# Kernel tuning notes

Measured on AMD Instinct MI355X. Metric: run time of the kernel, lower is better.

## Reference

```python
import jax, jax.numpy as jnp
from jax import lax
import numpy as np

N_TOOLS = 50
DIM = 512
N_TOKENS = 8192
PARAM_DIM = 256


def setup_inputs() -> dict:
    key = jax.random.key(0)
    ks = jax.random.split(key, 8)
    s = 1.0 / np.sqrt(DIM)
    x = jax.random.normal(ks[0], (N_TOKENS, DIM), dtype=jnp.float32)
    router_w = jax.random.uniform(ks[1], (N_TOOLS, DIM), jnp.float32, -s, s)
    router_b = jax.random.uniform(ks[2], (N_TOOLS,), jnp.float32, -s, s)
    expert_w = jax.random.uniform(ks[3], (N_TOOLS, DIM, DIM), jnp.float32, -s, s)
    expert_b = jax.random.uniform(ks[4], (N_TOOLS, DIM), jnp.float32, -s, s)
    param_w = jax.random.uniform(ks[5], (PARAM_DIM, DIM), jnp.float32, -s, s)
    param_b = jax.random.uniform(ks[6], (PARAM_DIM,), jnp.float32, -s, s)
    return {"x": x, "router_w": router_w, "router_b": router_b,
            "expert_w": expert_w, "expert_b": expert_b,
            "param_w": param_w, "param_b": param_b}


def _moe_adapt(x, tool_idx, expert_w, expert_b):
    # Top-1 dispatch: for each expert i, y_i = x @ W_i.T + b_i, written only
    # where tool_idx == i. Scan over the fixed 50 experts (mirrors the torch
    # masked per-expert Linear loop) with masked select instead of scatter.
    def step(acc, wb):
        i, W, b = wb
        y = x @ W.T + b  # [N, dim]
        mask = (tool_idx == i)[:, None]
        return jnp.where(mask, y, acc), None

    init = jnp.zeros_like(x)
    acc, _ = lax.scan(step, init, (jnp.arange(N_TOOLS), expert_w, expert_b))
    return acc


def reference(x, router_w, router_b, expert_w, expert_b, param_w, param_b):
    tool_logits = x @ router_w.T + router_b            # [N, 50]
    tool_probs = jax.nn.softmax(tool_logits, axis=-1)   # [N, 50]
    tool_idx = jnp.argmax(tool_probs, axis=-1)          # [N] int
    adapted = _moe_adapt(x, tool_idx, expert_w, expert_b)  # [N, dim]
    params = x @ param_w.T + param_b                    # [N, 256]
    return (tool_idx, tool_probs, adapted, params)
```

## Files before the change

kernel.cpp:

```cpp
#include <hip/hip_runtime.h>
#include <hip/hip_bf16.h>
#include <math.h>

#define N_TOKENS 8192
#define DIM      512
#define N_TOOLS  50
#define PARAM_DIM 256
#define N_ROWBLK (N_TOKENS / 64)
#define MAX_BATCHES 128
#define TM 128
#define LDSS 72

typedef float  f32x4 __attribute__((ext_vector_type(4)));
typedef short  s16x8 __attribute__((ext_vector_type(8)));
typedef short  s16x4 __attribute__((ext_vector_type(4)));

#define WS_IDX     0
#define WS_COUNTS  8192
#define WS_CURSOR  8256
#define WS_OFFSETS 8320
#define WS_BE      8384
#define WS_BM0     8512
#define WS_NB      8640
#define WS_ORDER   8704
#define WS_PWH     16896
#define WS_RWH     82432
#define WS_RWL     98816
#define WS_XH      115200
#define WS_XL      2212352

__device__ inline float bf2f(short s) {
    return __uint_as_float(((unsigned)(unsigned short)s) << 16);
}

__device__ inline s16x4 pk4(float a, float b, float c, float d) {
    __hip_bfloat162 p0 = __float22bfloat162_rn(make_float2(a, b));
    __hip_bfloat162 p1 = __float22bfloat162_rn(make_float2(c, d));
    union { __hip_bfloat162 h; short2 s; } u0, u1;
    u0.h = p0; u1.h = p1;
    s16x4 r; r[0] = u0.s.x; r[1] = u0.s.y; r[2] = u1.s.x; r[3] = u1.s.y;
    return r;
}

#define CVT_XB  4096
#define CVT_PWB 128
#define CVT_RWB 32
#define CVT_GRID (CVT_XB + CVT_PWB + CVT_RWB + 1)
__global__ __launch_bounds__(256) void cvt_kernel(const float* __restrict__ x,
                                                  const float* __restrict__ pw,
                                                  const float* __restrict__ rw,
                                                  short* __restrict__ xh,
                                                  short* __restrict__ xl,
                                                  short* __restrict__ pwh,
                                                  short* __restrict__ rwh,
                                                  short* __restrict__ rwl,
                                                  int* __restrict__ counts) {
    int bid = blockIdx.x;
    int tid = threadIdx.x;
    if (bid < CVT_XB) {
        size_t i = ((size_t)bid * 256 + tid) * 4;
        float4 v = *(const float4*)&x[i];
        s16x4 h = pk4(v.x, v.y, v.z, v.w);
        s16x4 l = pk4(v.x - bf2f(h[0]), v.y - bf2f(h[1]),
                      v.z - bf2f(h[2]), v.w - bf2f(h[3]));
        *(s16x4*)&xh[i] = h;
        *(s16x4*)&xl[i] = l;
    } else if (bid < CVT_XB + CVT_PWB) {
        size_t i = ((size_t)(bid - CVT_XB) * 256 + tid) * 4;
        float4 v = *(const float4*)&pw[i];
        *(s16x4*)&pwh[i] = pk4(v.x, v.y, v.z, v.w);
    } else if (bid < CVT_XB + CVT_PWB + CVT_RWB) {
        int i = ((bid - CVT_XB - CVT_PWB) * 256 + tid) * 4;
        int row = i >> 9;
        float4 v = {0.f, 0.f, 0.f, 0.f};
        if (row < N_TOOLS) v = *(const float4*)&rw[i];
        s16x4 h = pk4(v.x, v.y, v.z, v.w);
        s16x4 l = pk4(v.x - bf2f(h[0]), v.y - bf2f(h[1]),
                      v.z - bf2f(h[2]), v.w - bf2f(h[3]));
        *(s16x4*)&rwh[i] = h;
        *(s16x4*)&rwl[i] = l;
    } else {
        if (tid < 64) counts[tid] = 0;
    }
}

__global__ __launch_bounds__(256) void head_mfma(const short* __restrict__ xh,
                                                 const short* __restrict__ xl,
                                                 const short* __restrict__ pwh,
                                                 const float* __restrict__ pb,
                                                 const short* __restrict__ rwh,
                                                 const short* __restrict__ rwl,
                                                 const float* __restrict__ rb,
                                                 float* __restrict__ out_params,
                                                 float* __restrict__ probs,
                                                 float* __restrict__ out_idx,
                                                 int* __restrict__ idx_i,
                                                 int* __restrict__ counts) {
    int r0 = blockIdx.y * 64;
    bool isl = (blockIdx.x == 4);
    int c0 = isl ? 0 : blockIdx.x * 64;

    __shared__ short As[64 * LDSS];
    __shared__ short Bs[64 * LDSS];
    __shared__ short Al[64 * LDSS];
    __shared__ short Bl[64 * LDSS];
    __shared__ int rowcol[64];

    int tid = threadIdx.x;
    int wv = tid >> 6;
    int lane = tid & 63;
    int fm = lane & 15;
    int q = lane >> 4;

    int ar0 = tid >> 3, ag = tid & 7;
    int ar1 = ar0 + 32;
    const short* aptr0 = xh + (size_t)(r0 + ar0) * DIM + ag * 8;
    const short* aptr1 = xh + (size_t)(r0 + ar1) * DIM + ag * 8;
    const short* alptr0 = xl + (size_t)(r0 + ar0) * DIM + ag * 8;
    const short* alptr1 = xl + (size_t)(r0 + ar1) * DIM + ag * 8;

    const short* bsrc = isl ? rwh : (pwh + (size_t)c0 * DIM);
    int bc[2], bg[2];
    const short* bph[2];
    const short* bpl[2];
#pragma unroll
    for (int i = 0; i < 2; ++i) {
        int u = i * 256 + tid;
        bc[i] = u >> 3; bg[i] = u & 7;
        bph[i] = bsrc + (size_t)bc[i] * DIM + bg[i] * 8;
        bpl[i] = rwl + (size_t)bc[i] * DIM + bg[i] * 8;
    }

    f32x4 acc[4] = {{0.f, 0.f, 0.f, 0.f}, {0.f, 0.f, 0.f, 0.f},
                    {0.f, 0.f, 0.f, 0.f}, {0.f, 0.f, 0.f, 0.f}};

    s16x8 apre0, apre1, alpre0, alpre1;
    s16x8 bpre[2], blpre[2];
    apre0 = *(const s16x8*)aptr0;
    apre1 = *(const s16x8*)aptr1;
    if (isl) { alpre0 = *(const s16x8*)alptr0; alpre1 = *(const s16x8*)alptr1; }
#pragma unroll
    for (int i = 0; i < 2; ++i) {
        bpre[i] = *(const s16x8*)bph[i];
        if (isl) blpre[i] = *(const s16x8*)bpl[i];
    }

    for (int k0 = 0; k0 < DIM; k0 += 64) {
        *(s16x8*)&As[ar0 * LDSS + ag * 8] = apre0;
        *(s16x8*)&As[ar1 * LDSS + ag * 8] = apre1;
#pragma unroll
        for (int i = 0; i < 2; ++i)
            *(s16x8*)&Bs[bc[i] * LDSS + bg[i] * 8] = bpre[i];
        if (isl) {
            *(s16x8*)&Al[ar0 * LDSS + ag * 8] = alpre0;
            *(s16x8*)&Al[ar1 * LDSS + ag * 8] = alpre1;
#pragma unroll
            for (int i = 0; i < 2; ++i)
                *(s16x8*)&Bl[bc[i] * LDSS + bg[i] * 8] = blpre[i];
        }
        __syncthreads();

        int kn = k0 + 64;
        if (kn < DIM) {
            apre0 = *(const s16x8*)(aptr0 + kn);
            apre1 = *(const s16x8*)(aptr1 + kn);
            if (isl) {
                alpre0 = *(const s16x8*)(alptr0 + kn);
                alpre1 = *(const s16x8*)(alptr1 + kn);
            }
#pragma unroll
            for (int i = 0; i < 2; ++i) {
                bpre[i] = *(const s16x8*)(bph[i] + kn);
                if (isl) blpre[i] = *(const s16x8*)(bpl[i] + kn);
            }
        }

#pragma unroll
        for (int kk = 0; kk < 64; kk += 32) {
            int ao = (wv * 16 + fm) * LDSS + kk + q * 8;
            s16x8 a = *(const s16x8*)&As[ao];
            if (!isl) {
#pragma unroll
                for (int n = 0; n < 4; ++n) {
                    s16x8 b = *(const s16x8*)&Bs[(n * 16 + fm) * LDSS + kk + q * 8];
                    acc[n] = __builtin_amdgcn_mfma_f32_16x16x32_bf16(a, b, acc[n], 0, 0, 0);
                }
            } else {
                s16x8 al = *(const s16x8*)&Al[ao];
#pragma unroll
                for (int n = 0; n < 4; ++n) {
                    int bo = (n * 16 + fm) * LDSS + kk + q * 8;
                    s16x8 b  = *(const s16x8*)&Bs[bo];
                    s16x8 bl = *(const s16x8*)&Bl[bo];
                    acc[n] = __builtin_amdgcn_mfma_f32_16x16x32_bf16(a,  b,  acc[n], 0, 0, 0);
                    acc[n] = __builtin_amdgcn_mfma_f32_16x16x32_bf16(a,  bl, acc[n], 0, 0, 0);
                    acc[n] = __builtin_amdgcn_mfma_f32_16x16x32_bf16(al, b,  acc[n], 0, 0, 0);
                }
            }
        }
        __syncthreads();
    }

    if (!isl) {
        float bias[4];
#pragma unroll
        for (int n = 0; n < 4; ++n) bias[n] = pb[c0 + n * 16 + fm];
#pragma unroll
        for (int r = 0; r < 4; ++r) {
            int row = r0 + wv * 16 + q * 4 + r;
            float* op = out_params + (size_t)row * PARAM_DIM + c0;
#pragma unroll
            for (int n = 0; n < 4; ++n) op[n * 16 + fm] = acc[n][r] + bias[n];
        }
    } else {
        float rbv[4];
#pragma unroll
        for (int n = 0; n < 4; ++n) {
            int c = n * 16 + fm;
            rbv[n] = (c < N_TOOLS) ? rb[c] : 0.f;
        }
#pragma unroll
        for (int rr = 0; rr < 4; ++rr) {
            int row_l = wv * 16 + q * 4 + rr;
            int row = r0 + row_l;
            float v[4];
            float vmax = -INFINITY; int vcol = N_TOOLS;
#pragma unroll
            for (int n = 0; n < 4; ++n) {
                int c = n * 16 + fm;
                v[n] = acc[n][rr] + rbv[n];
                if (c < N_TOOLS && v[n] > vmax) { vmax = v[n]; vcol = c; }
            }
#pragma unroll
            for (int s = 1; s < 16; s <<= 1) {
                float om = __shfl_xor(vmax, s, 64);
                int   oc = __shfl_xor(vcol, s, 64);
                if (om > vmax || (om == vmax && oc < vcol)) { vmax = om; vcol = oc; }
            }
            float e[4]; float esum = 0.f;
#pragma unroll
            for (int n = 0; n < 4; ++n) {
                int c = n * 16 + fm;
                e[n] = (c < N_TOOLS) ? expf(v[n] - vmax) : 0.f;
                esum += e[n];
            }
#pragma unroll
            for (int s = 1; s < 16; s <<= 1) esum += __shfl_xor(esum, s, 64);
            float inv = 1.f / esum;
#pragma unroll
            for (int n = 0; n < 4; ++n) {
                int c = n * 16 + fm;
                if (c < N_TOOLS) probs[(size_t)row * N_TOOLS + c] = e[n] * inv;
            }
            if (fm == 0) {
                out_idx[row] = (float)vcol;
                idx_i[row] = vcol;
                rowcol[row_l] = vcol;
            }
        }
        __syncthreads();
        if (wv == 0) {
            int myc = rowcol[lane];
            int cnt = 0;
            for (int e2 = 0; e2 < N_TOOLS; ++e2) {
                unsigned long long m = __ballot(myc == e2);
                if (lane == e2) cnt = __popcll(m);
            }
            if (lane < N_TOOLS && cnt > 0) atomicAdd(&counts[lane], cnt);
        }
    }
}

__global__ void plumb_kernel(const int* __restrict__ counts,
                             int* __restrict__ offsets,
                             int* __restrict__ cursor,
                             int* __restrict__ batch_e,
                             int* __restrict__ batch_m0,
                             int* __restrict__ nb_out) {
    int lane = threadIdx.x;
    int c = (lane < N_TOOLS) ? counts[lane] : 0;
    int pre = c;
#pragma unroll
    for (int s = 1; s < 64; s <<= 1) {
        int v = __shfl_up(pre, s, 64);
        if (lane >= s) pre += v;
    }
    if (lane < N_TOOLS) { offsets[lane] = pre - c; cursor[lane] = pre - c; }

    int nb_i = (lane < N_TOOLS) ? (c + TM - 1) / TM : 0;
    int pre2 = nb_i;
#pragma unroll
    for (int s = 1; s < 64; s <<= 1) {
        int v = __shfl_up(pre2, s, 64);
        if (lane >= s) pre2 += v;
    }
    int bstart = pre2 - nb_i;
    for (int b = 0; b < nb_i; ++b) {
        batch_e[bstart + b] = lane;
        batch_m0[bstart + b] = b * TM;
    }
    if (lane == 63) nb_out[0] = pre2;
}

__global__ __launch_bounds__(256) void reorder_kernel(const int* __restrict__ idx_i,
                                                      int* __restrict__ cursor,
                                                      int* __restrict__ order) {
    __shared__ int lcnt[N_TOOLS];
    __shared__ int lbase[N_TOOLS];
    int tid = threadIdx.x;
    if (tid < N_TOOLS) lcnt[tid] = 0;
    __syncthreads();
    int t = blockIdx.x * 256 + tid;
    int e = idx_i[t];
    int r = atomicAdd(&lcnt[e], 1);
    __syncthreads();
    if (tid < N_TOOLS && lcnt[tid] > 0) lbase[tid] = atomicAdd(&cursor[tid], lcnt[tid]);
    __syncthreads();
    order[lbase[e] + r] = t;
}

__global__ __launch_bounds__(256) void adapted_mfma(const short* __restrict__ xh,
                                                    const float* __restrict__ ew,
                                                    const float* __restrict__ eb,
                                                    const int* __restrict__ order,
                                                    const int* __restrict__ batch_e,
                                                    const int* __restrict__ batch_m0,
                                                    const int* __restrict__ nb_ptr,
                                                    const int* __restrict__ offsets,
                                                    const int* __restrict__ counts,
                                                    float* __restrict__ out) {
    int b = blockIdx.y;
    if (b >= nb_ptr[0]) return;
    int e = batch_e[b];
    int m0 = batch_m0[b];
    int c0 = blockIdx.x * 64;
    int start = offsets[e] + m0;
    int len = counts[e] - m0;
    if (len > TM) len = TM;

    __shared__ short As[TM * LDSS];
    __shared__ short Bs[64 * LDSS];
    __shared__ int toks[TM];

    int tid = threadIdx.x;
    if (tid < TM) toks[tid] = (tid < len) ? order[start + tid] : -1;
    __syncthreads();

    int wv = tid >> 6;
    int lane = tid & 63;
    int fm = lane & 15;
    int q = lane >> 4;

    const float* We = ew + (size_t)e * DIM * DIM;

    int ag = tid & 7;
    int ar[4]; const short* aptr[4];
#pragma unroll
    for (int i = 0; i < 4; ++i) {
        ar[i] = i * 32 + (tid >> 3);
        int tk = toks[ar[i]];
        aptr[i] = (tk >= 0) ? xh + (size_t)tk * DIM + ag * 8 : nullptr;
    }
    int bc[4], bg[4];
    const float* bptr[4];
#pragma unroll
    for (int i = 0; i < 4; ++i) {
        int u = i * 256 + tid;
        bc[i] = u >> 4; bg[i] = u & 15;
        bptr[i] = We + (size_t)(c0 + bc[i]) * DIM + bg[i] * 4;
    }

    f32x4 acc[8] = {{0.f,0.f,0.f,0.f},{0.f,0.f,0.f,0.f},{0.f,0.f,0.f,0.f},{0.f,0.f,0.f,0.f},
                    {0.f,0.f,0.f,0.f},{0.f,0.f,0.f,0.f},{0.f,0.f,0.f,0.f},{0.f,0.f,0.f,0.f}};

    const s16x8 z8 = {0, 0, 0, 0, 0, 0, 0, 0};
    s16x8 apre[4];
    float4 bpre[4];
#pragma unroll
    for (int i = 0; i < 4; ++i) apre[i] = aptr[i] ? *(const s16x8*)aptr[i] : z8;
#pragma unroll
    for (int i = 0; i < 4; ++i) bpre[i] = *(const float4*)bptr[i];

    for (int k0 = 0; k0 < DIM; k0 += 64) {
#pragma unroll
        for (int i = 0; i < 4; ++i)
            *(s16x8*)&As[ar[i] * LDSS + ag * 8] = apre[i];
#pragma unroll
        for (int i = 0; i < 4; ++i) {
            float4 v = bpre[i];
            *(s16x4*)&Bs[bc[i] * LDSS + bg[i] * 4] = pk4(v.x, v.y, v.z, v.w);
        }
        __syncthreads();

        int kn = k0 + 64;
        if (kn < DIM) {
#pragma unroll
            for (int i = 0; i < 4; ++i) apre[i] = aptr[i] ? *(const s16x8*)(aptr[i] + kn) : z8;
#pragma unroll
            for (int i = 0; i < 4; ++i) bpre[i] = *(const float4*)(bptr[i] + kn);
        }

#pragma unroll
        for (int kk = 0; kk < 64; kk += 32) {
            s16x8 a0 = *(const s16x8*)&As[(wv * 32 + fm) * LDSS + kk + q * 8];
            s16x8 a1 = *(const s16x8*)&As[(wv * 32 + 16 + fm) * LDSS + kk + q * 8];
#pragma unroll
            for (int n = 0; n < 4; ++n) {
                s16x8 bf = *(const s16x8*)&Bs[(n * 16 + fm) * LDSS + kk + q * 8];
                acc[n]     = __builtin_amdgcn_mfma_f32_16x16x32_bf16(a0, bf, acc[n],     0, 0, 0);
                acc[4 + n] = __builtin_amdgcn_mfma_f32_16x16x32_bf16(a1, bf, acc[4 + n], 0, 0, 0);
            }
        }
        __syncthreads();
    }

    float bias[4];
#pragma unroll
    for (int n = 0; n < 4; ++n) bias[n] = eb[(size_t)e * DIM + c0 + n * 16 + fm];

#pragma unroll
    for (int m = 0; m < 2; ++m) {
#pragma unroll
        for (int r = 0; r < 4; ++r) {
            int row = wv * 32 + m * 16 + q * 4 + r;
            int tok = toks[row];
            if (tok < 0) continue;
            float* op = out + (size_t)tok * DIM + c0;
#pragma unroll
            for (int n = 0; n < 4; ++n) op[n * 16 + fm] = acc[m * 4 + n][r] + bias[n];
        }
    }
}

extern "C" void kernel_launch(void* const* d_in, const int* in_sizes, int n_in,
                              void* d_out, int out_size, void* d_ws, size_t ws_size,
                              hipStream_t stream) {
    const float* x        = (const float*)d_in[0];
    const float* router_w = (const float*)d_in[1];
    const float* router_b = (const float*)d_in[2];
    const float* expert_w = (const float*)d_in[3];
    const float* expert_b = (const float*)d_in[4];
    const float* param_w  = (const float*)d_in[5];
    const float* param_b  = (const float*)d_in[6];

    float* out = (float*)d_out;
    float* out_idx     = out;
    float* out_probs   = out + N_TOKENS;
    float* out_adapted = out + N_TOKENS + N_TOKENS * N_TOOLS;
    float* out_params  = out_adapted + (size_t)N_TOKENS * DIM;

    int* ws = (int*)d_ws;
    int* ws_idx     = ws + WS_IDX;
    int* ws_counts  = ws + WS_COUNTS;
    int* ws_cursor  = ws + WS_CURSOR;
    int* ws_offsets = ws + WS_OFFSETS;
    int* ws_be      = ws + WS_BE;
    int* ws_bm0     = ws + WS_BM0;
    int* ws_nb      = ws + WS_NB;
    int* ws_order   = ws + WS_ORDER;
    short* ws_pwh   = (short*)(ws + WS_PWH);
    short* ws_rwh   = (short*)(ws + WS_RWH);
    short* ws_rwl   = (short*)(ws + WS_RWL);
    short* ws_xh    = (short*)(ws + WS_XH);
    short* ws_xl    = (short*)(ws + WS_XL);

    cvt_kernel<<<CVT_GRID, 256, 0, stream>>>(x, param_w, router_w,
                                             ws_xh, ws_xl, ws_pwh, ws_rwh, ws_rwl,
                                             ws_counts);

    head_mfma<<<dim3(5, N_ROWBLK), 256, 0, stream>>>(ws_xh, ws_xl, ws_pwh, param_b,
                                                     ws_rwh, ws_rwl, router_b,
                                                     out_params, out_probs,
                                                     out_idx, ws_idx, ws_counts);

    plumb_kernel<<<1, 64, 0, stream>>>(ws_counts, ws_offsets, ws_cursor,
                                       ws_be, ws_bm0, ws_nb);

    reorder_kernel<<<N_TOKENS / 256, 256, 0, stream>>>(ws_idx, ws_cursor, ws_order);

    adapted_mfma<<<dim3(8, MAX_BATCHES), 256, 0, stream>>>(ws_xh, expert_w, expert_b,
                                                           ws_order, ws_be, ws_bm0, ws_nb,
                                                           ws_offsets, ws_counts, out_adapted);
}
```

Measured before the change: 152.3 us.

## Fuse x conversion into head GEMM, single-block sort, larger expert tiles

The standalone x-to-bf16 hi/lo conversion pass is removed. The head kernel now reads fp32 x directly, converts it in registers, computes the lo part only for the router tile, and writes the bf16 x copy from one column tile. Counting, prefix and reorder collapse into one 1024-thread sort kernel that uses ballot ranks, replacing the atomics plus the plumb and reorder kernels. The expert GEMM tile grows to 256 rows with 16 accumulators per wave, and both grids are remapped for XCD locality. The sort now runs in a single block, and the bigger tiles add register pressure and padding work for small experts.

```diff
diff --git a/kernel.cpp b/kernel.cpp
--- a/kernel.cpp
+++ b/kernel.cpp
@@ -7,8 +7,8 @@
 #define N_TOOLS  50
 #define PARAM_DIM 256
 #define N_ROWBLK (N_TOKENS / 64)
-#define MAX_BATCHES 128
-#define TM 128
+#define MAX_BATCHES 96
+#define TM 256
 #define LDSS 72
 
 typedef float  f32x4 __attribute__((ext_vector_type(4)));
@@ -16,18 +16,16 @@
 typedef short  s16x4 __attribute__((ext_vector_type(4)));
 
 #define WS_IDX     0
-#define WS_COUNTS  8192
-#define WS_CURSOR  8256
-#define WS_OFFSETS 8320
-#define WS_BE      8384
-#define WS_BM0     8512
-#define WS_NB      8640
-#define WS_ORDER   8704
-#define WS_PWH     16896
-#define WS_RWH     82432
-#define WS_RWL     98816
-#define WS_XH      115200
-#define WS_XL      2212352
+#define WS_OFFSETS 8192
+#define WS_COUNTS  8256
+#define WS_BE      8320
+#define WS_BM0     8416
+#define WS_NB      8512
+#define WS_ORDER   8528
+#define WS_PWH     16720
+#define WS_RWH     82256
+#define WS_RWL     98640
+#define WS_XH      115024
 
 __device__ inline float bf2f(short s) {
     return __uint_as_float(((unsigned)(unsigned short)s) << 16);
@@ -42,35 +40,42 @@
     return r;
 }
 
-#define CVT_XB  4096
+__device__ inline s16x8 pk8(float4 a, float4 b) {
+    s16x4 lo = pk4(a.x, a.y, a.z, a.w);
+    s16x4 hi = pk4(b.x, b.y, b.z, b.w);
+    s16x8 r;
+    r[0] = lo[0]; r[1] = lo[1]; r[2] = lo[2]; r[3] = lo[3];
+    r[4] = hi[0]; r[5] = hi[1]; r[6] = hi[2]; r[7] = hi[3];
+    return r;
+}
+
+__device__ inline s16x8 pk8lo(float4 a, float4 b, s16x8 h) {
+    s16x4 lo = pk4(a.x - bf2f(h[0]), a.y - bf2f(h[1]),
+                   a.z - bf2f(h[2]), a.w - bf2f(h[3]));
+    s16x4 hi = pk4(b.x - bf2f(h[4]), b.y - bf2f(h[5]),
+                   b.z - bf2f(h[6]), b.w - bf2f(h[7]));
+    s16x8 r;
+    r[0] = lo[0]; r[1] = lo[1]; r[2] = lo[2]; r[3] = lo[3];
+    r[4] = hi[0]; r[5] = hi[1]; r[6] = hi[2]; r[7] = hi[3];
+    return r;
+}
+
 #define CVT_PWB 128
 #define CVT_RWB 32
-#define CVT_GRID (CVT_XB + CVT_PWB + CVT_RWB + 1)
-__global__ __launch_bounds__(256) void cvt_kernel(const float* __restrict__ x,
-                                                  const float* __restrict__ pw,
-                                                  const float* __restrict__ rw,
-                                                  short* __restrict__ xh,
-                                                  short* __restrict__ xl,
-                                                  short* __restrict__ pwh,
-                                                  short* __restrict__ rwh,
-                                                  short* __restrict__ rwl,
-                                                  int* __restrict__ counts) {
+#define CVT_GRID (CVT_PWB + CVT_RWB)
+__global__ __launch_bounds__(256) void cvtB_kernel(const float* __restrict__ pw,
+                                                   const float* __restrict__ rw,
+                                                   short* __restrict__ pwh,
+                                                   short* __restrict__ rwh,
+                                                   short* __restrict__ rwl) {
     int bid = blockIdx.x;
     int tid = threadIdx.x;
-    if (bid < CVT_XB) {
+    if (bid < CVT_PWB) {
         size_t i = ((size_t)bid * 256 + tid) * 4;
-        float4 v = *(const float4*)&x[i];
-        s16x4 h = pk4(v.x, v.y, v.z, v.w);
-        s16x4 l = pk4(v.x - bf2f(h[0]), v.y - bf2f(h[1]),
-                      v.z - bf2f(h[2]), v.w - bf2f(h[3]));
-        *(s16x4*)&xh[i] = h;
-        *(s16x4*)&xl[i] = l;
-    } else if (bid < CVT_XB + CVT_PWB) {
-        size_t i = ((size_t)(bid - CVT_XB) * 256 + tid) * 4;
         float4 v = *(const float4*)&pw[i];
         *(s16x4*)&pwh[i] = pk4(v.x, v.y, v.z, v.w);
-    } else if (bid < CVT_XB + CVT_PWB + CVT_RWB) {
-        int i = ((bid - CVT_XB - CVT_PWB) * 256 + tid) * 4;
+    } else {
+        int i = ((bid - CVT_PWB) * 256 + tid) * 4;
         int row = i >> 9;
         float4 v = {0.f, 0.f, 0.f, 0.f};
         if (row < N_TOOLS) v = *(const float4*)&rw[i];
@@ -79,13 +84,10 @@
                       v.z - bf2f(h[2]), v.w - bf2f(h[3]));
         *(s16x4*)&rwh[i] = h;
         *(s16x4*)&rwl[i] = l;
-    } else {
-        if (tid < 64) counts[tid] = 0;
-    }
-}
-
-__global__ __launch_bounds__(256) void head_mfma(const short* __restrict__ xh,
-                                                 const short* __restrict__ xl,
+    }
+}
+
+__global__ __launch_bounds__(256) void head_mfma(const float* __restrict__ x,
                                                  const short* __restrict__ pwh,
                                                  const float* __restrict__ pb,
                                                  const short* __restrict__ rwh,
@@ -95,16 +97,22 @@
                                                  float* __restrict__ probs,
                                                  float* __restrict__ out_idx,
                                                  int* __restrict__ idx_i,
-                                                 int* __restrict__ counts) {
-    int r0 = blockIdx.y * 64;
-    bool isl = (blockIdx.x == 4);
-    int c0 = isl ? 0 : blockIdx.x * 64;
+                                                 short* __restrict__ xh) {
+    int bid = blockIdx.x;
+    int xcd = bid & 7;
+    int g = bid >> 3;
+    int tl = g % 5;
+    int yy = (g / 5) * 8 + xcd;
+
+    int r0 = yy * 64;
+    bool isl = (tl == 4);
+    bool isw = (tl == 0);
+    int c0 = isl ? 0 : tl * 64;
 
     __shared__ short As[64 * LDSS];
     __shared__ short Bs[64 * LDSS];
     __shared__ short Al[64 * LDSS];
     __shared__ short Bl[64 * LDSS];
-    __shared__ int rowcol[64];
 
     int tid = threadIdx.x;
     int wv = tid >> 6;
@@ -114,10 +122,10 @@
 
     int ar0 = tid >> 3, ag = tid & 7;
     int ar1 = ar0 + 32;
-    const short* aptr0 = xh + (size_t)(r0 + ar0) * DIM + ag * 8;
-    const short* aptr1 = xh + (size_t)(r0 + ar1) * DIM + ag * 8;
-    const short* alptr0 = xl + (size_t)(r0 + ar0) * DIM + ag * 8;
-    const short* alptr1 = xl + (size_t)(r0 + ar1) * DIM + ag * 8;
+    const float* xp0 = x + (size_t)(r0 + ar0) * DIM + ag * 8;
+    const float* xp1 = x + (size_t)(r0 + ar1) * DIM + ag * 8;
+    short* xo0 = xh + (size_t)(r0 + ar0) * DIM + ag * 8;
+    short* xo1 = xh + (size_t)(r0 + ar1) * DIM + ag * 8;
 
     const short* bsrc = isl ? rwh : (pwh + (size_t)c0 * DIM);
     int bc[2], bg[2];
@@ -134,11 +142,10 @@
     f32x4 acc[4] = {{0.f, 0.f, 0.f, 0.f}, {0.f, 0.f, 0.f, 0.f},
                     {0.f, 0.f, 0.f, 0.f}, {0.f, 0.f, 0.f, 0.f}};
 
-    s16x8 apre0, apre1, alpre0, alpre1;
+    float4 xa0, xb0, xa1, xb1;
     s16x8 bpre[2], blpre[2];
-    apre0 = *(const s16x8*)aptr0;
-    apre1 = *(const s16x8*)aptr1;
-    if (isl) { alpre0 = *(const s16x8*)alptr0; alpre1 = *(const s16x8*)alptr1; }
+    xa0 = *(const float4*)xp0; xb0 = *(const float4*)(xp0 + 4);
+    xa1 = *(const float4*)xp1; xb1 = *(const float4*)(xp1 + 4);
 #pragma unroll
     for (int i = 0; i < 2; ++i) {
         bpre[i] = *(const s16x8*)bph[i];
@@ -146,14 +153,22 @@
     }
 
     for (int k0 = 0; k0 < DIM; k0 += 64) {
-        *(s16x8*)&As[ar0 * LDSS + ag * 8] = apre0;
-        *(s16x8*)&As[ar1 * LDSS + ag * 8] = apre1;
+        s16x8 h0 = pk8(xa0, xb0);
+        s16x8 h1 = pk8(xa1, xb1);
+        *(s16x8*)&As[ar0 * LDSS + ag * 8] = h0;
+        *(s16x8*)&As[ar1 * LDSS + ag * 8] = h1;
+        if (isl) {
+            *(s16x8*)&Al[ar0 * LDSS + ag * 8] = pk8lo(xa0, xb0, h0);
+            *(s16x8*)&Al[ar1 * LDSS + ag * 8] = pk8lo(xa1, xb1, h1);
+        }
+        if (isw) {
+            *(s16x8*)(xo0 + k0) = h0;
+            *(s16x8*)(xo1 + k0) = h1;
+        }
 #pragma unroll
         for (int i = 0; i < 2; ++i)
             *(s16x8*)&Bs[bc[i] * LDSS + bg[i] * 8] = bpre[i];
         if (isl) {
-            *(s16x8*)&Al[ar0 * LDSS + ag * 8] = alpre0;
-            *(s16x8*)&Al[ar1 * LDSS + ag * 8] = alpre1;
 #pragma unroll
             for (int i = 0; i < 2; ++i)
                 *(s16x8*)&Bl[bc[i] * LDSS + bg[i] * 8] = blpre[i];
@@ -162,12 +177,8 @@
 
         int kn = k0 + 64;
         if (kn < DIM) {
-            apre0 = *(const s16x8*)(aptr0 + kn);
-            apre1 = *(const s16x8*)(aptr1 + kn);
-            if (isl) {
-                alpre0 = *(const s16x8*)(alptr0 + kn);
-                alpre1 = *(const s16x8*)(alptr1 + kn);
-            }
+            xa0 = *(const float4*)(xp0 + kn); xb0 = *(const float4*)(xp0 + kn + 4);
+            xa1 = *(const float4*)(xp1 + kn); xb1 = *(const float4*)(xp1 + kn + 4);
 #pragma unroll
             for (int i = 0; i < 2; ++i) {
                 bpre[i] = *(const s16x8*)(bph[i] + kn);
@@ -221,8 +232,7 @@
         }
 #pragma unroll
         for (int rr = 0; rr < 4; ++rr) {
-            int row_l = wv * 16 + q * 4 + rr;
-            int row = r0 + row_l;
+            int row = r0 + wv * 16 + q * 4 + rr;
             float v[4];
             float vmax = -INFINITY; int vcol = N_TOOLS;
 #pragma unroll
@@ -255,68 +265,84 @@
             if (fm == 0) {
                 out_idx[row] = (float)vcol;
                 idx_i[row] = vcol;
-                rowcol[row_l] = vcol;
-            }
-        }
-        __syncthreads();
-        if (wv == 0) {
-            int myc = rowcol[lane];
-            int cnt = 0;
-            for (int e2 = 0; e2 < N_TOOLS; ++e2) {
-                unsigned long long m = __ballot(myc == e2);
-                if (lane == e2) cnt = __popcll(m);
-            }
-            if (lane < N_TOOLS && cnt > 0) atomicAdd(&counts[lane], cnt);
-        }
-    }
-}
-
-__global__ void plumb_kernel(const int* __restrict__ counts,
-                             int* __restrict__ offsets,
-                             int* __restrict__ cursor,
-                             int* __restrict__ batch_e,
-                             int* __restrict__ batch_m0,
-                             int* __restrict__ nb_out) {
-    int lane = threadIdx.x;
-    int c = (lane < N_TOOLS) ? counts[lane] : 0;
-    int pre = c;
-#pragma unroll
-    for (int s = 1; s < 64; s <<= 1) {
-        int v = __shfl_up(pre, s, 64);
-        if (lane >= s) pre += v;
-    }
-    if (lane < N_TOOLS) { offsets[lane] = pre - c; cursor[lane] = pre - c; }
-
-    int nb_i = (lane < N_TOOLS) ? (c + TM - 1) / TM : 0;
-    int pre2 = nb_i;
-#pragma unroll
-    for (int s = 1; s < 64; s <<= 1) {
-        int v = __shfl_up(pre2, s, 64);
-        if (lane >= s) pre2 += v;
-    }
-    int bstart = pre2 - nb_i;
-    for (int b = 0; b < nb_i; ++b) {
-        batch_e[bstart + b] = lane;
-        batch_m0[bstart + b] = b * TM;
-    }
-    if (lane == 63) nb_out[0] = pre2;
-}
-
-__global__ __launch_bounds__(256) void reorder_kernel(const int* __restrict__ idx_i,
-                                                      int* __restrict__ cursor,
-                                                      int* __restrict__ order) {
-    __shared__ int lcnt[N_TOOLS];
-    __shared__ int lbase[N_TOOLS];
+            }
+        }
+    }
+}
+
+__global__ __launch_bounds__(1024) void sort_kernel(const int* __restrict__ idx,
+                                                    int* __restrict__ offsets,
+                                                    int* __restrict__ counts,
+                                                    int* __restrict__ order,
+                                                    int* __restrict__ batch_e,
+                                                    int* __restrict__ batch_m0,
+                                                    int* __restrict__ nb_out) {
+    __shared__ int cnt[128][N_TOOLS];
+    __shared__ int offs[64];
     int tid = threadIdx.x;
-    if (tid < N_TOOLS) lcnt[tid] = 0;
+    int w = tid >> 6;
+    int lane = tid & 63;
+    unsigned long long lt = (1ull << lane) - 1ull;
+
+    int myE[8], myRank[8];
+#pragma unroll
+    for (int r = 0; r < 8; ++r) {
+        int t = w * 512 + r * 64 + lane;
+        int e = idx[t];
+        myE[r] = e;
+        int rank = 0, c = 0;
+        for (int ex = 0; ex < N_TOOLS; ++ex) {
+            unsigned long long m = __ballot(e == ex);
+            if (e == ex) rank = __popcll(m & lt);
+            if (lane == ex) c = __popcll(m);
+        }
+        myRank[r] = rank;
+        if (lane < N_TOOLS) cnt[w * 8 + r][lane] = c;
+    }
     __syncthreads();
-    int t = blockIdx.x * 256 + tid;
-    int e = idx_i[t];
-    int r = atomicAdd(&lcnt[e], 1);
+
+    if (tid < 64) {
+        int base = 0;
+        if (tid < N_TOOLS) {
+            for (int i = 0; i < 128; ++i) {
+                int tmp = cnt[i][tid];
+                cnt[i][tid] = base;
+                base += tmp;
+            }
+        }
+        int c = base;
+        int pre = c;
+#pragma unroll
+        for (int s = 1; s < 64; s <<= 1) {
+            int v = __shfl_up(pre, s, 64);
+            if (tid >= s) pre += v;
+        }
+        int off = pre - c;
+        offs[tid] = off;
+        if (tid < N_TOOLS) { offsets[tid] = off; counts[tid] = c; }
+
+        int nb_i = (tid < N_TOOLS) ? (c + TM - 1) / TM : 0;
+        int pre2 = nb_i;
+#pragma unroll
+        for (int s = 1; s < 64; s <<= 1) {
+            int v = __shfl_up(pre2, s, 64);
+            if (tid >= s) pre2 += v;
+        }
+        int bstart = pre2 - nb_i;
+        for (int b = 0; b < nb_i; ++b) {
+            batch_e[bstart + b] = tid;
+            batch_m0[bstart + b] = b * TM;
+        }
+        if (tid == 63) nb_out[0] = pre2;
+    }
     __syncthreads();
-    if (tid < N_TOOLS && lcnt[tid] > 0) lbase[tid] = atomicAdd(&cursor[tid], lcnt[tid]);
-    __syncthreads();
-    order[lbase[e] + r] = t;
+
+#pragma unroll
+    for (int r = 0; r < 8; ++r) {
+        int t = w * 512 + r * 64 + lane;
+        int e = myE[r];
+        order[offs[e] + cnt[w * 8 + r][e] + myRank[r]] = t;
+    }
 }
 
 __global__ __launch_bounds__(256) void adapted_mfma(const short* __restrict__ xh,
@@ -329,11 +355,15 @@
                                                     const int* __restrict__ offsets,
                                                     const int* __restrict__ counts,
                                                     float* __restrict__ out) {
-    int b = blockIdx.y;
+    int bid = blockIdx.x;
+    int x8 = bid & 7;
+    int u = bid >> 3;
+    int ct = u & 7;
+    int b = (bid >> 6) * 8 + x8;
     if (b >= nb_ptr[0]) return;
     int e = batch_e[b];
     int m0 = batch_m0[b];
-    int c0 = blockIdx.x * 64;
+    int c0 = ct * 64;
     int start = offsets[e] + m0;
     int len = counts[e] - m0;
     if (len > TM) len = TM;
@@ -343,7 +373,7 @@
     __shared__ int toks[TM];
 
     int tid = threadIdx.x;
-    if (tid < TM) toks[tid] = (tid < len) ? order[start + tid] : -1;
+    toks[tid] = (tid < len) ? order[start + tid] : -1;
     __syncthreads();
 
     int wv = tid >> 6;
@@ -354,37 +384,38 @@
     const float* We = ew + (size_t)e * DIM * DIM;
 
     int ag = tid & 7;
-    int ar[4]; const short* aptr[4];
-#pragma unroll
-    for (int i = 0; i < 4; ++i) {
-        ar[i] = i * 32 + (tid >> 3);
-        int tk = toks[ar[i]];
+    int arr = tid >> 3;
+    const short* aptr[8];
+#pragma unroll
+    for (int i = 0; i < 8; ++i) {
+        int tk = toks[i * 32 + arr];
         aptr[i] = (tk >= 0) ? xh + (size_t)tk * DIM + ag * 8 : nullptr;
     }
     int bc[4], bg[4];
     const float* bptr[4];
 #pragma unroll
     for (int i = 0; i < 4; ++i) {
-        int u = i * 256 + tid;
-        bc[i] = u >> 4; bg[i] = u & 15;
+        int u2 = i * 256 + tid;
+        bc[i] = u2 >> 4; bg[i] = u2 & 15;
         bptr[i] = We + (size_t)(c0 + bc[i]) * DIM + bg[i] * 4;
     }
 
-    f32x4 acc[8] = {{0.f,0.f,0.f,0.f},{0.f,0.f,0.f,0.f},{0.f,0.f,0.f,0.f},{0.f,0.f,0.f,0.f},
-                    {0.f,0.f,0.f,0.f},{0.f,0.f,0.f,0.f},{0.f,0.f,0.f,0.f},{0.f,0.f,0.f,0.f}};
+    f32x4 acc[16];
+#pragma unroll
+    for (int i = 0; i < 16; ++i) acc[i] = (f32x4){0.f, 0.f, 0.f, 0.f};
 
     const s16x8 z8 = {0, 0, 0, 0, 0, 0, 0, 0};
-    s16x8 apre[4];
+    s16x8 apre[8];
     float4 bpre[4];
 #pragma unroll
-    for (int i = 0; i < 4; ++i) apre[i] = aptr[i] ? *(const s16x8*)aptr[i] : z8;
+    for (int i = 0; i < 8; ++i) apre[i] = aptr[i] ? *(const s16x8*)aptr[i] : z8;
 #pragma unroll
     for (int i = 0; i < 4; ++i) bpre[i] = *(const float4*)bptr[i];
 
     for (int k0 = 0; k0 < DIM; k0 += 64) {
 #pragma unroll
-        for (int i = 0; i < 4; ++i)
-            *(s16x8*)&As[ar[i] * LDSS + ag * 8] = apre[i];
+        for (int i = 0; i < 8; ++i)
+            *(s16x8*)&As[(i * 32 + arr) * LDSS + ag * 8] = apre[i];
 #pragma unroll
         for (int i = 0; i < 4; ++i) {
             float4 v = bpre[i];
@@ -395,20 +426,23 @@
         int kn = k0 + 64;
         if (kn < DIM) {
 #pragma unroll
-            for (int i = 0; i < 4; ++i) apre[i] = aptr[i] ? *(const s16x8*)(aptr[i] + kn) : z8;
+            for (int i = 0; i < 8; ++i) apre[i] = aptr[i] ? *(const s16x8*)(aptr[i] + kn) : z8;
 #pragma unroll
             for (int i = 0; i < 4; ++i) bpre[i] = *(const float4*)(bptr[i] + kn);
         }
 
 #pragma unroll
         for (int kk = 0; kk < 64; kk += 32) {
-            s16x8 a0 = *(const s16x8*)&As[(wv * 32 + fm) * LDSS + kk + q * 8];
-            s16x8 a1 = *(const s16x8*)&As[(wv * 32 + 16 + fm) * LDSS + kk + q * 8];
+            s16x8 a[4];
+#pragma unroll
+            for (int m = 0; m < 4; ++m)
+                a[m] = *(const s16x8*)&As[(wv * 64 + m * 16 + fm) * LDSS + kk + q * 8];
 #pragma unroll
             for (int n = 0; n < 4; ++n) {
-                s16x8 bf = *(const s16x8*)&Bs[(n * 16 + fm) * LDSS + kk + q * 8];
-                acc[n]     = __builtin_amdgcn_mfma_f32_16x16x32_bf16(a0, bf, acc[n],     0, 0, 0);
-                acc[4 + n] = __builtin_amdgcn_mfma_f32_16x16x32_bf16(a1, bf, acc[4 + n], 0, 0, 0);
+                s16x8 bfv = *(const s16x8*)&Bs[(n * 16 + fm) * LDSS + kk + q * 8];
+#pragma unroll
+                for (int m = 0; m < 4; ++m)
+                    acc[n * 4 + m] = __builtin_amdgcn_mfma_f32_16x16x32_bf16(a[m], bfv, acc[n * 4 + m], 0, 0, 0);
             }
         }
         __syncthreads();
@@ -419,15 +453,15 @@
     for (int n = 0; n < 4; ++n) bias[n] = eb[(size_t)e * DIM + c0 + n * 16 + fm];
 
 #pragma unroll
-    for (int m = 0; m < 2; ++m) {
+    for (int m = 0; m < 4; ++m) {
 #pragma unroll
         for (int r = 0; r < 4; ++r) {
-            int row = wv * 32 + m * 16 + q * 4 + r;
+            int row = wv * 64 + m * 16 + q * 4 + r;
             int tok = toks[row];
             if (tok < 0) continue;
             float* op = out + (size_t)tok * DIM + c0;
 #pragma unroll
-            for (int n = 0; n < 4; ++n) op[n * 16 + fm] = acc[m * 4 + n][r] + bias[n];
+            for (int n = 0; n < 4; ++n) op[n * 16 + fm] = acc[n * 4 + m][r] + bias[n];
         }
     }
 }
@@ -451,9 +485,8 @@
 
     int* ws = (int*)d_ws;
     int* ws_idx     = ws + WS_IDX;
+    int* ws_offsets = ws + WS_OFFSETS;
     int* ws_counts  = ws + WS_COUNTS;
-    int* ws_cursor  = ws + WS_CURSOR;
-    int* ws_offsets = ws + WS_OFFSETS;
     int* ws_be      = ws + WS_BE;
     int* ws_bm0     = ws + WS_BM0;
     int* ws_nb      = ws + WS_NB;
@@ -462,23 +495,16 @@
     short* ws_rwh   = (short*)(ws + WS_RWH);
     short* ws_rwl   = (short*)(ws + WS_RWL);
     short* ws_xh    = (short*)(ws + WS_XH);
-    short* ws_xl    = (short*)(ws + WS_XL);
-
-    cvt_kernel<<<CVT_GRID, 256, 0, stream>>>(x, param_w, router_w,
-                                             ws_xh, ws_xl, ws_pwh, ws_rwh, ws_rwl,
-                                             ws_counts);
-
-    head_mfma<<<dim3(5, N_ROWBLK), 256, 0, stream>>>(ws_xh, ws_xl, ws_pwh, param_b,
-                                                     ws_rwh, ws_rwl, router_b,
-                                                     out_params, out_probs,
-                                                     out_idx, ws_idx, ws_counts);
-
-    plumb_kernel<<<1, 64, 0, stream>>>(ws_counts, ws_offsets, ws_cursor,
-                                       ws_be, ws_bm0, ws_nb);
-
-    reorder_kernel<<<N_TOKENS / 256, 256, 0, stream>>>(ws_idx, ws_cursor, ws_order);
-
-    adapted_mfma<<<dim3(8, MAX_BATCHES), 256, 0, stream>>>(ws_xh, expert_w, expert_b,
-                                                           ws_order, ws_be, ws_bm0, ws_nb,
-                                                           ws_offsets, ws_counts, out_adapted);
-}
+
+    cvtB_kernel<<<CVT_GRID, 256, 0, stream>>>(param_w, router_w, ws_pwh, ws_rwh, ws_rwl);
+
+    head_mfma<<<640, 256, 0, stream>>>(x, ws_pwh, param_b, ws_rwh, ws_rwl, router_b,
+                                       out_params, out_probs, out_idx, ws_idx, ws_xh);
+
+    sort_kernel<<<1, 1024, 0, stream>>>(ws_idx, ws_offsets, ws_counts, ws_order,
+                                        ws_be, ws_bm0, ws_nb);
+
+    adapted_mfma<<<768, 256, 0, stream>>>(ws_xh, expert_w, expert_b,
+                                          ws_order, ws_be, ws_bm0, ws_nb,
+                                          ws_offsets, ws_counts, out_adapted);
+}
```

After: 181.5 us. 19.1% more time.
